# Kernel tuning notes

Hardware: AMD Instinct MI355X
Metric: run time of the kernel (lower is better)

Reference implementation:

```python
import jax, jax.numpy as jnp
import numpy as np

N_NODES = 100000
E2 = 1600000
E3 = 1600000
ES = 100000
HID = 64


def _mlp_3x3(x_in, W1, b1, W2, b2):
    # x_in: [E, d_in] -> mobility [E, 3, 3]
    h = jax.nn.relu(x_in @ W1 + b1)
    out = h @ W2 + b2  # [E, 9]
    return out.reshape(-1, 3, 3)


def setup_inputs() -> dict:
    key = jax.random.key(0)
    ks = jax.random.split(key, 20)
    inp = {}
    inp["x"] = jax.random.normal(ks[0], (N_NODES, 3), dtype=jnp.float32)
    inp["edge_2body"] = jax.random.randint(ks[1], (2, E2), 0, N_NODES)
    inp["edge_3body"] = jax.random.randint(ks[2], (3, E3), 0, N_NODES)
    inp["edge_2bodySelf"] = jax.random.randint(ks[3], (2, ES), 0, N_NODES)
    inp["edge_1body"] = jax.random.randint(ks[4], (2, ES), 0, N_NODES)
    inp["edge_attr_2body"] = jax.random.normal(ks[5], (E2, 3), dtype=jnp.float32)
    inp["edge_attr_3body"] = jax.random.normal(ks[6], (E3, 3), dtype=jnp.float32)
    inp["edge_attr_2bodySelf"] = jax.random.normal(ks[7], (ES, 3), dtype=jnp.float32)
    inp["edge_attr_1body"] = jax.random.normal(ks[8], (ES, 3), dtype=jnp.float32)
    s = 0.1
    # nn_2body: 3 -> HID -> 9
    inp["W1_2b"] = jax.random.normal(ks[9], (3, HID), dtype=jnp.float32) * s
    inp["b1_2b"] = jnp.zeros((HID,), jnp.float32)
    inp["W2_2b"] = jax.random.normal(ks[10], (HID, 9), dtype=jnp.float32) * s
    inp["b2_2b"] = jnp.zeros((9,), jnp.float32)
    # nn_3body: 6 -> HID -> 9
    inp["W1_3b"] = jax.random.normal(ks[11], (6, HID), dtype=jnp.float32) * s
    inp["b1_3b"] = jnp.zeros((HID,), jnp.float32)
    inp["W2_3b"] = jax.random.normal(ks[12], (HID, 9), dtype=jnp.float32) * s
    inp["b2_3b"] = jnp.zeros((9,), jnp.float32)
    # nn_self: 3 -> HID -> 9
    inp["W1_s"] = jax.random.normal(ks[13], (3, HID), dtype=jnp.float32) * s
    inp["b1_s"] = jnp.zeros((HID,), jnp.float32)
    inp["W2_s"] = jax.random.normal(ks[14], (HID, 9), dtype=jnp.float32) * s
    inp["b2_s"] = jnp.zeros((9,), jnp.float32)
    return inp


def reference(x, edge_2body, edge_3body, edge_2bodySelf, edge_1body,
              edge_attr_2body, edge_attr_3body, edge_attr_2bodySelf, edge_attr_1body,
              W1_2b, b1_2b, W2_2b, b2_2b,
              W1_3b, b1_3b, W2_3b, b2_3b,
              W1_s, b1_s, W2_s, b2_s):
    n = x.shape[0]
    # ---- 2-body: gather -> MLP -> per-edge 3x3 matvec -> scatter-add ----
    d2 = x[edge_2body[0]] - x[edge_2body[1]]  # xj - xi, [E2,3]
    mob2 = _mlp_3x3(d2, W1_2b, b1_2b, W2_2b, b2_2b)
    y2 = jnp.einsum('eij,ej->ei', mob2, edge_attr_2body)
    v2 = jax.ops.segment_sum(y2, edge_2body[1], num_segments=n)
    # ---- 3-body ----
    xj = x[edge_3body[0]]
    xk = x[edge_3body[1]]
    xi = x[edge_3body[2]]
    d3 = jnp.concatenate((xk - xj, xi - xk), axis=1)  # [E3,6]
    mob3 = _mlp_3x3(d3, W1_3b, b1_3b, W2_3b, b2_3b)
    y3 = jnp.einsum('eij,ej->ei', mob3, edge_attr_3body)
    v3 = jax.ops.segment_sum(y3, edge_3body[2], num_segments=n)
    # ---- 2-body self ----
    ds = x[edge_2bodySelf[0]] - x[edge_2bodySelf[1]]
    mobs = _mlp_3x3(ds, W1_s, b1_s, W2_s, b2_s)
    ys = jnp.einsum('eij,ej->ei', mobs, edge_attr_2bodySelf)
    vs = jax.ops.segment_sum(ys, edge_2bodySelf[1], num_segments=n)
    # edge_1body / edge_attr_1body unused in original forward
    return v2 + v3 + vs
```

## Files before the change

kernel.cpp:

```cpp
#include <hip/hip_runtime.h>


constexpr int HIDDEN = 64;
constexpr int NB_MAX = 256;
constexpr int NPB_SHIFT = 9;
constexpr int NPB = 1 << NPB_SHIFT;
constexpr int SSPLIT = 8;
constexpr int TILE_F = NPB * 3;
constexpr int TILE_F4 = TILE_F / 4;
constexpr int NET_SLOT = 1024;

typedef _Float16 h2_t __attribute__((ext_vector_type(2)));

__device__ __forceinline__ unsigned packh2(float a, float b) {
    auto h = __builtin_amdgcn_cvt_pkrtz(a, b);
    return __builtin_bit_cast(unsigned, h);
}
__device__ __forceinline__ float fdot2u(unsigned a, unsigned b, float c) {
    h2_t ha = __builtin_bit_cast(h2_t, a);
    h2_t hb = __builtin_bit_cast(h2_t, b);
#if __has_builtin(__builtin_amdgcn_fdot2)
    return __builtin_amdgcn_fdot2(ha, hb, c, false);
#else
    return fmaf((float)ha.x, (float)hb.x, fmaf((float)ha.y, (float)hb.y, c));
#endif
}


__global__ __launch_bounds__(256) void setup_kernel(
    const float* __restrict__ x, int n_nodes, float4* __restrict__ x4,
    int* __restrict__ gcount,
    const float* __restrict__ W1_2b, const float* __restrict__ b1_2b,
    const float* __restrict__ W2_2b, const float* __restrict__ b2_2b,
    const float* __restrict__ W1_s,  const float* __restrict__ b1_s,
    const float* __restrict__ W2_s,  const float* __restrict__ b2_s,
    const float* __restrict__ W1_3b, const float* __restrict__ b1_3b,
    const float* __restrict__ W2_3b, const float* __restrict__ b2_3b,
    unsigned* __restrict__ nets)
{
    const int blk = blockIdx.x;
    const int tid = threadIdx.x;
    if (blk < 3) {
        const float *W1, *b1, *W2, *b2; int din;
        if (blk == 0) { W1 = W1_2b; b1 = b1_2b; W2 = W2_2b; b2 = b2_2b; din = 3; }
        else if (blk == 1) { W1 = W1_s; b1 = b1_s; W2 = W2_s; b2 = b2_s; din = 3; }
        else { W1 = W1_3b; b1 = b1_3b; W2 = W2_3b; b2 = b2_3b; din = 6; }
        unsigned* slot = nets + blk * NET_SLOT;
        float* slotf = (float*)slot;
        if (tid < 64) {
            int hh = tid;
            if (din == 3) {
                slot[hh] = packh2(W1[0 * HIDDEN + hh], W1[1 * HIDDEN + hh]);
                slotf[560 + hh] = W1[2 * HIDDEN + hh];
            } else {
                #pragma unroll
                for (int r = 0; r < 3; ++r)
                    slot[hh * 3 + r] =
                        packh2(W1[(2 * r) * HIDDEN + hh], W1[(2 * r + 1) * HIDDEN + hh]);
            }
            slotf[192 + hh] = b1[hh];
        }
        for (int t = tid; t < 288; t += 256) {
            int hh2 = t / 9, i = t - hh2 * 9;
            slot[256 + t] = packh2(W2[(2 * hh2) * 9 + i], W2[(2 * hh2 + 1) * 9 + i]);
        }
        if (tid < 9) slotf[544 + tid] = b2[tid];
        if (blk == 0) gcount[tid] = 0;
    } else {
        int i = (blk - 3) * 256 + tid;
        if (i < n_nodes)
            x4[i] = make_float4(x[3 * i], x[3 * i + 1], x[3 * i + 2], 0.0f);
    }
}

__global__ __launch_bounds__(256) void p1_edge_kernel(
    const float4* __restrict__ x4,
    const int* __restrict__ e0, long long E0, const float* __restrict__ at0,
    const int* __restrict__ e1, long long E1, const float* __restrict__ at1,
    const int* __restrict__ e2, long long E2, const float* __restrict__ at2,
    int g0, int g1,
    const unsigned* __restrict__ nets,
    float4* __restrict__ records, int* __restrict__ gcount, int cap)
{
    constexpr int BLK = 256;
    constexpr int KPT = 4;

    __shared__ int s_hist[NB_MAX];
    __shared__ int s_base[NB_MAX];
    __shared__ int s_rank[NB_MAX];

    const int blk = blockIdx.x;
    const int* edges; long long E; const float* attr;
    int bidx, nblk, din3;
    const unsigned* wp;
    if (blk < g0)           { edges = e0; E = E0; attr = at0; bidx = blk;          nblk = g0;                 din3 = 1; wp = nets; }
    else if (blk < g0 + g1) { edges = e1; E = E1; attr = at1; bidx = blk - g0;     nblk = g1;                 din3 = 1; wp = nets + NET_SLOT; }
    else                    { edges = e2; E = E2; attr = at2; bidx = blk - g0 - g1; nblk = gridDim.x - g0 - g1; din3 = 0; wp = nets + 2 * NET_SLOT; }
    const float* wpf = (const float*)wp;

    const int tid = threadIdx.x;
    const long long span = (E + nblk - 1) / nblk;
    const long long lo = (long long)bidx * span;
    const long long hi = (lo + span < E) ? (lo + span) : E;
    if (lo >= E) return;

    for (int i = tid; i < NB_MAX; i += BLK) { s_hist[i] = 0; s_rank[i] = 0; }
    __syncthreads();

    const long long dstrow = din3 ? E : 2 * E;
    for (long long e = lo + tid; e < hi; e += BLK) {
        int d = edges[dstrow + e];
        atomicAdd(&s_hist[d >> NPB_SHIFT], 1);
    }
    __syncthreads();

    for (int i = tid; i < NB_MAX; i += BLK) {
        int h = s_hist[i];
        s_base[i] = (h > 0) ? atomicAdd(&gcount[i], h) : 0;
    }
    __syncthreads();

    for (long long t0 = lo; t0 < hi; t0 += BLK * KPT) {
        unsigned dp[KPT][3];
        float    d2s[KPT];
        float    a[KPT][3];
        int      dst[KPT];
        bool     valid[KPT];

        #pragma unroll
        for (int u = 0; u < KPT; ++u) {
            long long e = t0 + (long long)u * BLK + tid;
            valid[u] = (e < hi);
            long long ee = valid[u] ? e : lo;
            if (din3) {
                int s = edges[ee];
                int t = edges[E + ee];
                dst[u] = t;
                float4 xs = x4[s];
                float4 xt = x4[t];
                dp[u][0] = packh2(xs.x - xt.x, xs.y - xt.y);
                d2s[u]   = xs.z - xt.z;
                dp[u][1] = 0; dp[u][2] = 0;
            } else {
                int j = edges[ee];
                int k = edges[E + ee];
                int i = edges[2 * E + ee];
                dst[u] = i;
                float4 xj = x4[j];
                float4 xk = x4[k];
                float4 xi = x4[i];
                dp[u][0] = packh2(xk.x - xj.x, xk.y - xj.y);
                dp[u][1] = packh2(xk.z - xj.z, xi.x - xk.x);
                dp[u][2] = packh2(xi.y - xk.y, xi.z - xk.z);
                d2s[u] = 0.f;
            }
            #pragma unroll
            for (int c = 0; c < 3; ++c) a[u][c] = attr[3 * ee + c];
        }

        float acc[KPT][9];
        #pragma unroll
        for (int u = 0; u < KPT; ++u)
            #pragma unroll
            for (int i = 0; i < 9; ++i) acc[u][i] = wpf[544 + i];

        if (din3) {
            #pragma unroll 2
            for (int hh2 = 0; hh2 < HIDDEN / 2; ++hh2) {
                const unsigned wA = wp[2 * hh2];
                const unsigned wB = wp[2 * hh2 + 1];
                const float wcA = wpf[560 + 2 * hh2];
                const float wcB = wpf[561 + 2 * hh2];
                const float bbA = wpf[192 + 2 * hh2];
                const float bbB = wpf[193 + 2 * hh2];
                unsigned w2p[9];
                #pragma unroll
                for (int i = 0; i < 9; ++i) w2p[i] = wp[256 + hh2 * 9 + i];
                #pragma unroll
                for (int u = 0; u < KPT; ++u) {
                    float preA = fmaf(d2s[u], wcA, fdot2u(dp[u][0], wA, bbA));
                    float preB = fmaf(d2s[u], wcB, fdot2u(dp[u][0], wB, bbB));
                    unsigned h2 = packh2(fmaxf(preA, 0.f), fmaxf(preB, 0.f));
                    #pragma unroll
                    for (int i = 0; i < 9; ++i)
                        acc[u][i] = fdot2u(h2, w2p[i], acc[u][i]);
                }
            }
        } else {
            #pragma unroll 2
            for (int hh2 = 0; hh2 < HIDDEN / 2; ++hh2) {
                const unsigned wA0 = wp[(2 * hh2) * 3 + 0];
                const unsigned wA1 = wp[(2 * hh2) * 3 + 1];
                const unsigned wA2 = wp[(2 * hh2) * 3 + 2];
                const unsigned wB0 = wp[(2 * hh2 + 1) * 3 + 0];
                const unsigned wB1 = wp[(2 * hh2 + 1) * 3 + 1];
                const unsigned wB2 = wp[(2 * hh2 + 1) * 3 + 2];
                const float bbA = wpf[192 + 2 * hh2];
                const float bbB = wpf[193 + 2 * hh2];
                unsigned w2p[9];
                #pragma unroll
                for (int i = 0; i < 9; ++i) w2p[i] = wp[256 + hh2 * 9 + i];
                #pragma unroll
                for (int u = 0; u < KPT; ++u) {
                    float preA = fdot2u(dp[u][2], wA2,
                                 fdot2u(dp[u][1], wA1,
                                 fdot2u(dp[u][0], wA0, bbA)));
                    float preB = fdot2u(dp[u][2], wB2,
                                 fdot2u(dp[u][1], wB1,
                                 fdot2u(dp[u][0], wB0, bbB)));
                    unsigned h2 = packh2(fmaxf(preA, 0.f), fmaxf(preB, 0.f));
                    #pragma unroll
                    for (int i = 0; i < 9; ++i)
                        acc[u][i] = fdot2u(h2, w2p[i], acc[u][i]);
                }
            }
        }

        #pragma unroll
        for (int u = 0; u < KPT; ++u) {
            if (!valid[u]) continue;
            float y0 = fmaf(acc[u][0], a[u][0], fmaf(acc[u][1], a[u][1], acc[u][2] * a[u][2]));
            float y1 = fmaf(acc[u][3], a[u][0], fmaf(acc[u][4], a[u][1], acc[u][5] * a[u][2]));
            float y2 = fmaf(acc[u][6], a[u][0], fmaf(acc[u][7], a[u][1], acc[u][8] * a[u][2]));
            int b = dst[u] >> NPB_SHIFT;
            int r = atomicAdd(&s_rank[b], 1);
            int slot = s_base[b] + r;
            if (slot < cap)
                records[(size_t)b * cap + slot] =
                    make_float4(y0, y1, y2, __int_as_float(dst[u]));
        }
    }
}

__global__ __launch_bounds__(256) void p2_partial(
    const float4* __restrict__ records, const int* __restrict__ gcount,
    int cap, float* __restrict__ partials)
{
    __shared__ float s_acc[TILE_F];
    const int b = blockIdx.x / SSPLIT;
    const int s = blockIdx.x % SSPLIT;
    const int tid = threadIdx.x;

    for (int i = tid; i < TILE_F; i += 256) s_acc[i] = 0.0f;
    __syncthreads();

    int cnt = gcount[b];
    if (cnt > cap) cnt = cap;
    const int chunk = (cnt + SSPLIT - 1) / SSPLIT;
    const int beg = s * chunk;
    const int end = min(beg + chunk, cnt);

    const float4* rb = records + (size_t)b * cap;
    for (int i = beg + tid; i < end; i += 256) {
        float4 r = rb[i];
        int loc = __float_as_int(r.w) - (b << NPB_SHIFT);
        atomicAdd(&s_acc[loc * 3 + 0], r.x);
        atomicAdd(&s_acc[loc * 3 + 1], r.y);
        atomicAdd(&s_acc[loc * 3 + 2], r.z);
    }
    __syncthreads();

    float* pt = partials + (size_t)blockIdx.x * TILE_F;
    for (int i = tid; i < TILE_F; i += 256) pt[i] = s_acc[i];
}

__global__ __launch_bounds__(256) void p2_final(
    const float4* __restrict__ partials, float4* __restrict__ out, int n4)
{
    int i4 = blockIdx.x * 256 + threadIdx.x;
    if (i4 >= n4) return;
    int b = i4 / TILE_F4;
    int loc = i4 - b * TILE_F4;
    const float4* base = partials + (size_t)b * SSPLIT * TILE_F4 + loc;
    float4 sum = base[0];
    #pragma unroll
    for (int s = 1; s < SSPLIT; ++s) {
        float4 v = base[(size_t)s * TILE_F4];
        sum.x += v.x; sum.y += v.y; sum.z += v.z; sum.w += v.w;
    }
    out[i4] = sum;
}

__global__ void p2_final_tail(const float* __restrict__ partials,
                              float* __restrict__ out, int start, int n)
{
    int idx = start + blockIdx.x * 64 + threadIdx.x;
    if (idx >= n) return;
    int b = idx / TILE_F;
    int loc = idx - b * TILE_F;
    const float* base = partials + (size_t)b * SSPLIT * TILE_F + loc;
    float sum = 0.f;
    #pragma unroll
    for (int s = 0; s < SSPLIT; ++s) sum += base[(size_t)s * TILE_F];
    out[idx] = sum;
}

template <int DIN, int KPT>
__global__ __launch_bounds__(256) void edge_mlp_atomic(
    const float* __restrict__ x,
    const int* __restrict__ edges, long long E,
    const float* __restrict__ attr,
    const float* __restrict__ W1, const float* __restrict__ b1,
    const float* __restrict__ W2, const float* __restrict__ b2,
    float* __restrict__ out)
{
    const int tid = threadIdx.x;
    const long long base = (long long)blockIdx.x * (blockDim.x * KPT) + tid;
    float d[KPT][DIN]; float a[KPT][3]; int dst[KPT]; bool valid[KPT];
    #pragma unroll
    for (int u = 0; u < KPT; ++u) {
        long long e = base + (long long)u * blockDim.x;
        valid[u] = (e < E);
        long long ee = valid[u] ? e : 0;
        if constexpr (DIN == 3) {
            int s = edges[ee]; int t = edges[E + ee]; dst[u] = t;
            #pragma unroll
            for (int c = 0; c < 3; ++c)
                d[u][c] = x[3 * (long long)s + c] - x[3 * (long long)t + c];
        } else {
            int j = edges[ee]; int k = edges[E + ee]; int i = edges[2 * E + ee];
            dst[u] = i;
            #pragma unroll
            for (int c = 0; c < 3; ++c) {
                float xj = x[3 * (long long)j + c];
                float xk = x[3 * (long long)k + c];
                float xi = x[3 * (long long)i + c];
                d[u][c] = xk - xj; d[u][3 + c] = xi - xk;
            }
        }
        #pragma unroll
        for (int c = 0; c < 3; ++c) a[u][c] = attr[3 * ee + c];
    }
    float acc[KPT][9];
    #pragma unroll
    for (int u = 0; u < KPT; ++u)
        #pragma unroll
        for (int i = 0; i < 9; ++i) acc[u][i] = b2[i];
    #pragma unroll 4
    for (int hh = 0; hh < HIDDEN; ++hh) {
        const float bb = b1[hh];
        float w1r[DIN];
        #pragma unroll
        for (int r = 0; r < DIN; ++r) w1r[r] = W1[r * HIDDEN + hh];
        float w2r[9];
        #pragma unroll
        for (int i = 0; i < 9; ++i) w2r[i] = W2[hh * 9 + i];
        #pragma unroll
        for (int u = 0; u < KPT; ++u) {
            float pre = bb;
            #pragma unroll
            for (int r = 0; r < DIN; ++r) pre = fmaf(d[u][r], w1r[r], pre);
            const float h = fmaxf(pre, 0.0f);
            #pragma unroll
            for (int i = 0; i < 9; ++i) acc[u][i] = fmaf(h, w2r[i], acc[u][i]);
        }
    }
    #pragma unroll
    for (int u = 0; u < KPT; ++u) {
        if (!valid[u]) continue;
        float* o = out + 3 * (long long)dst[u];
        #pragma unroll
        for (int i = 0; i < 3; ++i) {
            float y = fmaf(acc[u][3 * i + 0], a[u][0],
                      fmaf(acc[u][3 * i + 1], a[u][1],
                           acc[u][3 * i + 2] * a[u][2]));
            atomicAdd(&o[i], y);
        }
    }
}

extern "C" void kernel_launch(void* const* d_in, const int* in_sizes, int n_in,
                              void* d_out, int out_size, void* d_ws, size_t ws_size,
                              hipStream_t stream)
{
    const float* x  = (const float*)d_in[0];
    const int*   e2 = (const int*)d_in[1];
    const int*   e3 = (const int*)d_in[2];
    const int*   es = (const int*)d_in[3];
    const float* a2 = (const float*)d_in[5];
    const float* a3 = (const float*)d_in[6];
    const float* as = (const float*)d_in[7];
    const float* W1_2b = (const float*)d_in[9];
    const float* b1_2b = (const float*)d_in[10];
    const float* W2_2b = (const float*)d_in[11];
    const float* b2_2b = (const float*)d_in[12];
    const float* W1_3b = (const float*)d_in[13];
    const float* b1_3b = (const float*)d_in[14];
    const float* W2_3b = (const float*)d_in[15];
    const float* b2_3b = (const float*)d_in[16];
    const float* W1_s  = (const float*)d_in[17];
    const float* b1_s  = (const float*)d_in[18];
    const float* W2_s  = (const float*)d_in[19];
    const float* b2_s  = (const float*)d_in[20];

    const long long E2 = in_sizes[1] / 2;
    const long long E3 = in_sizes[2] / 3;
    const long long ES = in_sizes[3] / 2;
    const long long Etot = E2 + E3 + ES;
    const int n_nodes = out_size / 3;
    const int nbuckets = (n_nodes + NPB - 1) >> NPB_SHIFT;

    float* out = (float*)d_out;

    const size_t off_nets = 1024;
    const size_t off_x4 = off_nets + 3 * NET_SLOT * 4;
    const size_t x4_bytes = (size_t)n_nodes * sizeof(float4);
    const size_t off_part = (off_x4 + x4_bytes + 255) & ~(size_t)255;
    const size_t part_bytes = (size_t)nbuckets * SSPLIT * TILE_F * sizeof(float);
    const size_t off_rec = off_part + part_bytes;

    long long mean_per_bucket = (Etot + nbuckets - 1) / nbuckets;
    long long min_cap = mean_per_bucket + 1600;
    long long cap_avail =
        ((long long)ws_size - (long long)off_rec) / ((long long)nbuckets * 16);

    constexpr int SPAN = 2048;
    int g0 = (int)((E2 + SPAN - 1) / SPAN);
    int g1 = (int)((ES + SPAN - 1) / SPAN);
    int g2g = (int)((E3 + SPAN - 1) / SPAN);

    if (nbuckets <= NB_MAX && cap_avail >= min_cap) {
        long long capL = min_cap + 4096;
        if (capL > cap_avail) capL = cap_avail;
        int cap = (int)capL;
        int* gcount = (int*)d_ws;
        unsigned* nets = (unsigned*)((char*)d_ws + off_nets);
        float4* x4 = (float4*)((char*)d_ws + off_x4);
        float* partials = (float*)((char*)d_ws + off_part);
        float4* records = (float4*)((char*)d_ws + off_rec);

        int nb_pad = (n_nodes + 255) / 256;
        setup_kernel<<<3 + nb_pad, 256, 0, stream>>>(
            x, n_nodes, x4, gcount,
            W1_2b, b1_2b, W2_2b, b2_2b,
            W1_s,  b1_s,  W2_s,  b2_s,
            W1_3b, b1_3b, W2_3b, b2_3b,
            nets);

        p1_edge_kernel<<<g0 + g1 + g2g, 256, 0, stream>>>(
            x4,
            e2, E2, a2,
            es, ES, as,
            e3, E3, a3,
            g0, g1,
            nets, records, gcount, cap);

        p2_partial<<<nbuckets * SSPLIT, 256, 0, stream>>>(records, gcount, cap, partials);

        int n4 = out_size / 4;
        int tail = out_size - n4 * 4;
        if (n4 > 0)
            p2_final<<<(n4 + 255) / 256, 256, 0, stream>>>(
                (const float4*)partials, (float4*)out, n4);
        if (tail > 0)
            p2_final_tail<<<1, 64, 0, stream>>>(partials, out, n4 * 4, out_size);
    } else {
        hipMemsetAsync(out, 0, (size_t)out_size * sizeof(float), stream);
        constexpr int BLK = 256, KPT = 4;
        const long long per_blk = (long long)BLK * KPT;
        int a2g = (int)((E2 + per_blk - 1) / per_blk);
        int a3g = (int)((E3 + per_blk - 1) / per_blk);
        int asg = (int)((ES + per_blk - 1) / per_blk);
        if (a2g > 0)
            edge_mlp_atomic<3, KPT><<<a2g, BLK, 0, stream>>>(
                x, e2, E2, a2, W1_2b, b1_2b, W2_2b, b2_2b, out);
        if (a3g > 0)
            edge_mlp_atomic<6, KPT><<<a3g, BLK, 0, stream>>>(
                x, e3, E3, a3, W1_3b, b1_3b, W2_3b, b2_3b, out);
        if (asg > 0)
            edge_mlp_atomic<3, KPT><<<asg, BLK, 0, stream>>>(
                x, es, ES, as, W1_s, b1_s, W2_s, b2_s, out);
    }
}
```

Baseline: 345.1 us.

## Software-pipeline edge gathers in p1 and use nontemporal loads/stores

The per-edge loop in the edge kernel now prefetches the next tile's edge indices, node coordinates and attributes into registers while the MLP runs on the current tile, with KPT reduced from 4 to 2 to limit register pressure. Streaming edge/attribute reads and record writes/reads use nontemporal builtins to avoid polluting cache, and the per-block edge span doubles so fewer blocks launch. The aim is to hide gather latency behind compute. The costs are extra live registers, which may lower occupancy, and less parallelism from fewer blocks.

```diff
diff --git a/kernel.cpp b/kernel.cpp
--- a/kernel.cpp
+++ b/kernel.cpp
@@ -11,6 +11,7 @@
 constexpr int NET_SLOT = 1024;
 
 typedef _Float16 h2_t __attribute__((ext_vector_type(2)));
+typedef float f32x4 __attribute__((ext_vector_type(4)));
 
 __device__ __forceinline__ unsigned packh2(float a, float b) {
     auto h = __builtin_amdgcn_cvt_pkrtz(a, b);
@@ -83,11 +84,14 @@
     float4* __restrict__ records, int* __restrict__ gcount, int cap)
 {
     constexpr int BLK = 256;
-    constexpr int KPT = 4;
+    constexpr int KPT = 2;
+    constexpr int TILE = BLK * KPT;
 
     __shared__ int s_hist[NB_MAX];
     __shared__ int s_base[NB_MAX];
     __shared__ int s_rank[NB_MAX];
+
+    const f32x4* xv = reinterpret_cast<const f32x4*>(x4);
 
     const int blk = blockIdx.x;
     const int* edges; long long E; const float* attr;
@@ -109,7 +113,7 @@
 
     const long long dstrow = din3 ? E : 2 * E;
     for (long long e = lo + tid; e < hi; e += BLK) {
-        int d = edges[dstrow + e];
+        int d = __builtin_nontemporal_load(edges + dstrow + e);
         atomicAdd(&s_hist[d >> NPB_SHIFT], 1);
     }
     __syncthreads();
@@ -120,49 +124,75 @@
     }
     __syncthreads();
 
-    for (long long t0 = lo; t0 < hi; t0 += BLK * KPT) {
+    int   rdst[KPT]; bool rval[KPT];
+    f32x4 rxa[KPT], rxb[KPT], rxc[KPT];
+    float rat[KPT][3];
+
+    auto load_tile = [&](long long t0) {
+        #pragma unroll
+        for (int u = 0; u < KPT; ++u) {
+            long long e = t0 + (long long)u * BLK + tid;
+            bool v = (e < hi);
+            long long ee = v ? e : lo;
+            rval[u] = v;
+            if (din3) {
+                int s = __builtin_nontemporal_load(edges + ee);
+                int t = __builtin_nontemporal_load(edges + E + ee);
+                rdst[u] = t;
+                rxa[u] = xv[s];
+                rxb[u] = xv[t];
+            } else {
+                int j = __builtin_nontemporal_load(edges + ee);
+                int k = __builtin_nontemporal_load(edges + E + ee);
+                int i = __builtin_nontemporal_load(edges + 2 * E + ee);
+                rdst[u] = i;
+                rxa[u] = xv[j];
+                rxb[u] = xv[k];
+                rxc[u] = xv[i];
+            }
+            #pragma unroll
+            for (int c = 0; c < 3; ++c)
+                rat[u][c] = __builtin_nontemporal_load(attr + 3 * ee + c);
+        }
+    };
+
+    float b2r[9];
+    #pragma unroll
+    for (int i = 0; i < 9; ++i) b2r[i] = wpf[544 + i];
+
+    load_tile(lo);
+
+    for (long long t0 = lo; t0 < hi; t0 += TILE) {
         unsigned dp[KPT][3];
         float    d2s[KPT];
         float    a[KPT][3];
         int      dst[KPT];
         bool     valid[KPT];
-
         #pragma unroll
         for (int u = 0; u < KPT; ++u) {
-            long long e = t0 + (long long)u * BLK + tid;
-            valid[u] = (e < hi);
-            long long ee = valid[u] ? e : lo;
+            valid[u] = rval[u];
+            dst[u] = rdst[u];
+            #pragma unroll
+            for (int c = 0; c < 3; ++c) a[u][c] = rat[u][c];
             if (din3) {
-                int s = edges[ee];
-                int t = edges[E + ee];
-                dst[u] = t;
-                float4 xs = x4[s];
-                float4 xt = x4[t];
-                dp[u][0] = packh2(xs.x - xt.x, xs.y - xt.y);
-                d2s[u]   = xs.z - xt.z;
+                dp[u][0] = packh2(rxa[u].x - rxb[u].x, rxa[u].y - rxb[u].y);
+                d2s[u]   = rxa[u].z - rxb[u].z;
                 dp[u][1] = 0; dp[u][2] = 0;
             } else {
-                int j = edges[ee];
-                int k = edges[E + ee];
-                int i = edges[2 * E + ee];
-                dst[u] = i;
-                float4 xj = x4[j];
-                float4 xk = x4[k];
-                float4 xi = x4[i];
-                dp[u][0] = packh2(xk.x - xj.x, xk.y - xj.y);
-                dp[u][1] = packh2(xk.z - xj.z, xi.x - xk.x);
-                dp[u][2] = packh2(xi.y - xk.y, xi.z - xk.z);
+                dp[u][0] = packh2(rxb[u].x - rxa[u].x, rxb[u].y - rxa[u].y);
+                dp[u][1] = packh2(rxb[u].z - rxa[u].z, rxc[u].x - rxb[u].x);
+                dp[u][2] = packh2(rxc[u].y - rxb[u].y, rxc[u].z - rxb[u].z);
                 d2s[u] = 0.f;
             }
-            #pragma unroll
-            for (int c = 0; c < 3; ++c) a[u][c] = attr[3 * ee + c];
-        }
+        }
+
+        if (t0 + TILE < hi) load_tile(t0 + TILE);
 
         float acc[KPT][9];
         #pragma unroll
         for (int u = 0; u < KPT; ++u)
             #pragma unroll
-            for (int i = 0; i < 9; ++i) acc[u][i] = wpf[544 + i];
+            for (int i = 0; i < 9; ++i) acc[u][i] = b2r[i];
 
         if (din3) {
             #pragma unroll 2
@@ -225,9 +255,13 @@
             int b = dst[u] >> NPB_SHIFT;
             int r = atomicAdd(&s_rank[b], 1);
             int slot = s_base[b] + r;
-            if (slot < cap)
-                records[(size_t)b * cap + slot] =
-                    make_float4(y0, y1, y2, __int_as_float(dst[u]));
+            if (slot < cap) {
+                f32x4 rec;
+                rec.x = y0; rec.y = y1; rec.z = y2;
+                rec.w = __int_as_float(dst[u]);
+                __builtin_nontemporal_store(
+                    rec, (f32x4*)&records[(size_t)b * cap + slot]);
+            }
         }
     }
 }
@@ -250,9 +284,9 @@
     const int beg = s * chunk;
     const int end = min(beg + chunk, cnt);
 
-    const float4* rb = records + (size_t)b * cap;
+    const f32x4* rb = (const f32x4*)(records + (size_t)b * cap);
     for (int i = beg + tid; i < end; i += 256) {
-        float4 r = rb[i];
+        f32x4 r = __builtin_nontemporal_load(rb + i);
         int loc = __float_as_int(r.w) - (b << NPB_SHIFT);
         atomicAdd(&s_acc[loc * 3 + 0], r.x);
         atomicAdd(&s_acc[loc * 3 + 1], r.y);
@@ -414,7 +448,7 @@
     long long cap_avail =
         ((long long)ws_size - (long long)off_rec) / ((long long)nbuckets * 16);
 
-    constexpr int SPAN = 2048;
+    constexpr int SPAN = 4096;
     int g0 = (int)((E2 + SPAN - 1) / SPAN);
     int g1 = (int)((ES + SPAN - 1) / SPAN);
     int g2g = (int)((E3 + SPAN - 1) / SPAN);
```

Result: slower. 452.0 us (+31.0%).
